# Kernel tuning notes

Measured on AMD Instinct MI355X. Metric: run time of the kernel, lower is better.

## Reference

```python
import jax, jax.numpy as jnp
import numpy as np

# irreps: 128x0e + 64x1o + 32x2e -> blocks of (mul, 2l+1)
MULS_LS = ((128, 0), (64, 1), (32, 2))
NODE_DIM = 128
NUM_IRREPS = 224  # 128+64+32
EQUI_DIM = 480    # 128*1 + 64*3 + 32*5
CONCAT = NODE_DIM + NUM_IRREPS  # 352
EPS = 1e-5
N = 100000


def _blocks(x):
    """Split flat equivariant feature [N, 480] into per-degree blocks [N, mul, 2l+1]."""
    outs, off = [], 0
    for mul, l in MULS_LS:
        d = 2 * l + 1
        outs.append(x[:, off:off + mul * d].reshape(x.shape[0], mul, d))
        off += mul * d
    return outs


def setup_inputs() -> dict:
    key = jax.random.key(0)
    k1, k2, k3, k4 = jax.random.split(key, 4)
    s = 1.0 / np.sqrt(CONCAT)
    return {
        "node_scalar": jax.random.normal(k1, (N, NODE_DIM), jnp.float32),
        "node_equi": jax.random.normal(k2, (N, EQUI_DIM), jnp.float32),
        "ln_w": jnp.ones((NODE_DIM,), jnp.float32),
        "ln_b": jnp.zeros((NODE_DIM,), jnp.float32),
        "W1": jax.random.normal(k3, (CONCAT, CONCAT), jnp.float32) * s,
        "b1": jnp.zeros((CONCAT,), jnp.float32),
        "W2": jax.random.normal(k4, (CONCAT, CONCAT), jnp.float32) * s,
        "b2": jnp.zeros((CONCAT,), jnp.float32),
    }


def reference(node_scalar, node_equi, ln_w, ln_b, W1, b1, W2, b2):
    # ---- scalar LayerNorm ----
    mu = node_scalar.mean(-1, keepdims=True)
    var = node_scalar.var(-1, keepdims=True)
    ns = (node_scalar - mu) * jax.lax.rsqrt(var + EPS) * ln_w + ln_b

    # ---- equivariant LayerNorm: per-degree, mean-centering for l=0, RMS of
    # per-channel norms over the multiplicity axis ----
    eb = []
    for (mul, l), blk in zip(MULS_LS, _blocks(node_equi)):
        if l == 0:
            blk = blk - blk.mean(axis=1, keepdims=True)
        norm2 = (blk * blk).sum(-1, keepdims=True).mean(axis=1, keepdims=True)
        eb.append(blk * jax.lax.rsqrt(norm2 + EPS))

    # ---- EquivariantDot(x, x): per-irrep self dot, component-normalized ----
    inv = jnp.concatenate(
        [(blk * blk).sum(-1) / np.sqrt(2 * l + 1) for (mul, l), blk in zip(MULS_LS, eb)],
        axis=-1)  # [N, 224]

    # ---- concat -> 2-layer gated MLP ----
    cat = jnp.concatenate([ns, inv], axis=-1)  # [N, 352]
    h = jax.nn.silu(cat @ W1 + b1) @ W2 + b2
    d_scalar, gate = h[:, :NODE_DIM], h[:, NODE_DIM:]

    # ---- ElementwiseTensorProduct(equi, gate 0e): per-irrep scalar gating ----
    gparts = jnp.split(gate, [128, 192], axis=-1)  # muls 128, 64, 32
    n = node_scalar.shape[0]
    d_equi = jnp.concatenate(
        [(blk * g[:, :, None]).reshape(n, -1) for blk, g in zip(eb, gparts)],
        axis=-1)  # [N, 480]

    # ---- residual update; concat outputs into one array [N, 608] ----
    return jnp.concatenate([node_scalar + d_scalar, node_equi + d_equi], axis=-1)
```

## Files before the change

### kernel.cpp

```cpp
#include <hip/hip_runtime.h>

#define NODE 128
#define EQUI 480
#define CATD 352
#define OUTD 608
#define RPB  32
#define SA   360
#define NTILES 22
#define KSTEPS 11
#define EPSF 1e-5f

typedef __bf16 bfv8 __attribute__((ext_vector_type(8)));
typedef float  f32x4 __attribute__((ext_vector_type(4)));

__device__ __forceinline__ unsigned short f2bf(float f) {
  unsigned int u = __builtin_bit_cast(unsigned int, f);
  u += 0x7FFFu + ((u >> 16) & 1u);
  return (unsigned short)(u >> 16);
}

__global__ void prep_kernel(const float* __restrict__ W1, const float* __restrict__ W2,
                            unsigned short* __restrict__ WT) {
  int idx = blockIdx.x * 256 + threadIdx.x;
  if (idx >= 2 * CATD * CATD) return;
  int which = (idx >= CATD * CATD);
  int rr = which ? idx - CATD * CATD : idx;
  int j = rr / CATD, k = rr - j * CATD;
  const float* W = which ? W2 : W1;
  WT[idx] = f2bf(W[k * CATD + j]);
}

__global__ __launch_bounds__(256, 2) void fused_kernel(
    const float* __restrict__ node_scalar, const float* __restrict__ node_equi,
    const float* __restrict__ ln_w, const float* __restrict__ ln_b,
    const unsigned short* __restrict__ W1T, const unsigned short* __restrict__ W2T,
    const float* __restrict__ b1, const float* __restrict__ b2,
    float* __restrict__ out, int N) {

  __shared__ __attribute__((aligned(16))) unsigned short sA[RPB * SA];
  __shared__ __attribute__((aligned(16))) unsigned short sH[RPB * SA];
  __shared__ float sMean0[RPB], sS0[RPB], sS1[RPB], sS2[RPB];

  const int tid  = threadIdx.x;
  const long row0 = (long)blockIdx.x * RPB;

  {
    const int r = tid >> 3, g = tid & 7;
    const long row_g = row0 + r;
    if (row_g < N) {
      float lv[16];
      float s = 0.f, q = 0.f;
      const float* xs = node_scalar + row_g * NODE;
      #pragma unroll
      for (int i = 0; i < 4; i++) {
        float4 t = *(const float4*)(xs + g * 16 + i * 4);
        lv[i*4+0] = t.x; lv[i*4+1] = t.y; lv[i*4+2] = t.z; lv[i*4+3] = t.w;
        s += t.x + t.y + t.z + t.w;
        q += t.x*t.x + t.y*t.y + t.z*t.z + t.w*t.w;
      }
      #pragma unroll
      for (int m = 1; m < 8; m <<= 1) { s += __shfl_xor(s, m, 64); q += __shfl_xor(q, m, 64); }
      float mean = s * (1.f / NODE);
      float rstd = rsqrtf(q * (1.f / NODE) - mean * mean + EPSF);
      #pragma unroll
      for (int i = 0; i < 16; i++) {
        int c = g * 16 + i;
        sA[r * SA + c] = f2bf((lv[i] - mean) * rstd * ln_w[c] + ln_b[c]);
      }
      const float* xe = node_equi + row_g * EQUI;
      s = 0.f; q = 0.f;
      #pragma unroll
      for (int i = 0; i < 4; i++) {
        float4 t = *(const float4*)(xe + g * 16 + i * 4);
        lv[i*4+0] = t.x; lv[i*4+1] = t.y; lv[i*4+2] = t.z; lv[i*4+3] = t.w;
        s += t.x + t.y + t.z + t.w;
        q += t.x*t.x + t.y*t.y + t.z*t.z + t.w*t.w;
      }
      #pragma unroll
      for (int m = 1; m < 8; m <<= 1) { s += __shfl_xor(s, m, 64); q += __shfl_xor(q, m, 64); }
      float mean0 = s * (1.f / 128.f);
      float s0 = rsqrtf(q * (1.f / 128.f) - mean0 * mean0 + EPSF);
      #pragma unroll
      for (int i = 0; i < 16; i++) {
        float e = (lv[i] - mean0) * s0;
        sA[r * SA + NODE + g * 16 + i] = f2bf(e * e);
      }
      if (g == 0) { sMean0[r] = mean0; sS0[r] = s0; }
      float a1[24]; q = 0.f;
      #pragma unroll
      for (int i = 0; i < 6; i++) {
        float4 t = *(const float4*)(xe + 128 + g * 24 + i * 4);
        a1[i*4+0] = t.x; a1[i*4+1] = t.y; a1[i*4+2] = t.z; a1[i*4+3] = t.w;
        q += t.x*t.x + t.y*t.y + t.z*t.z + t.w*t.w;
      }
      #pragma unroll
      for (int m = 1; m < 8; m <<= 1) q += __shfl_xor(q, m, 64);
      float s1 = rsqrtf(q * (1.f / 64.f) + EPSF);
      float s1q = s1 * s1 * 0.57735026919f;
      #pragma unroll
      for (int mi = 0; mi < 8; mi++) {
        float ss = a1[mi*3]*a1[mi*3] + a1[mi*3+1]*a1[mi*3+1] + a1[mi*3+2]*a1[mi*3+2];
        sA[r * SA + 256 + g * 8 + mi] = f2bf(ss * s1q);
      }
      if (g == 0) sS1[r] = s1;
      float a2[20]; q = 0.f;
      #pragma unroll
      for (int i = 0; i < 5; i++) {
        float4 t = *(const float4*)(xe + 320 + g * 20 + i * 4);
        a2[i*4+0] = t.x; a2[i*4+1] = t.y; a2[i*4+2] = t.z; a2[i*4+3] = t.w;
        q += t.x*t.x + t.y*t.y + t.z*t.z + t.w*t.w;
      }
      #pragma unroll
      for (int m = 1; m < 8; m <<= 1) q += __shfl_xor(q, m, 64);
      float s2 = rsqrtf(q * (1.f / 32.f) + EPSF);
      float s2q = s2 * s2 * 0.44721359549f;
      #pragma unroll
      for (int mi = 0; mi < 4; mi++) {
        float ss = a2[mi*5]*a2[mi*5] + a2[mi*5+1]*a2[mi*5+1] + a2[mi*5+2]*a2[mi*5+2]
                 + a2[mi*5+3]*a2[mi*5+3] + a2[mi*5+4]*a2[mi*5+4];
        sA[r * SA + 320 + g * 4 + mi] = f2bf(ss * s2q);
      }
      if (g == 0) sS2[r] = s2;
    }
  }
  __syncthreads();

  const int lane = tid & 63, wv = tid >> 6;
  const int ml = lane & 15, quad = lane >> 4;
  const int koff = quad * 8;

  for (int nt = wv; nt < NTILES; nt += 4) {
    f32x4 acc0  = {0.f, 0.f, 0.f, 0.f};
    f32x4 acc1  = {0.f, 0.f, 0.f, 0.f};
    f32x4 acc0b = {0.f, 0.f, 0.f, 0.f};
    f32x4 acc1b = {0.f, 0.f, 0.f, 0.f};
    const unsigned short* Bp = W1T + (nt * 16 + ml) * CATD + koff;
    const unsigned short* A0 = &sA[ml * SA + koff];
    const unsigned short* A1 = &sA[(ml + 16) * SA + koff];
    #pragma unroll
    for (int ks = 0; ks < KSTEPS; ks++) {
      bfv8 b  = *(const bfv8*)(Bp + ks * 32);
      bfv8 a0 = *(const bfv8*)(A0 + ks * 32);
      bfv8 a1 = *(const bfv8*)(A1 + ks * 32);
      if (ks & 1) {
        acc0b = __builtin_amdgcn_mfma_f32_16x16x32_bf16(a0, b, acc0b, 0, 0, 0);
        acc1b = __builtin_amdgcn_mfma_f32_16x16x32_bf16(a1, b, acc1b, 0, 0, 0);
      } else {
        acc0 = __builtin_amdgcn_mfma_f32_16x16x32_bf16(a0, b, acc0, 0, 0, 0);
        acc1 = __builtin_amdgcn_mfma_f32_16x16x32_bf16(a1, b, acc1, 0, 0, 0);
      }
    }
    acc0 += acc0b;
    acc1 += acc1b;
    const int col = nt * 16 + ml;
    const float bb = b1[col];
    #pragma unroll
    for (int reg = 0; reg < 4; reg++) {
      int rr = quad * 4 + reg;
      float v0 = acc0[reg] + bb; v0 = v0 / (1.f + __expf(-v0));
      sH[rr * SA + col] = f2bf(v0);
      float v1 = acc1[reg] + bb; v1 = v1 / (1.f + __expf(-v1));
      sH[(rr + 16) * SA + col] = f2bf(v1);
    }
  }
  __syncthreads();

  for (int nt = wv; nt < NTILES; nt += 4) {
    f32x4 acc0  = {0.f, 0.f, 0.f, 0.f};
    f32x4 acc1  = {0.f, 0.f, 0.f, 0.f};
    f32x4 acc0b = {0.f, 0.f, 0.f, 0.f};
    f32x4 acc1b = {0.f, 0.f, 0.f, 0.f};
    const unsigned short* Bp = W2T + (nt * 16 + ml) * CATD + koff;
    const unsigned short* A0 = &sH[ml * SA + koff];
    const unsigned short* A1 = &sH[(ml + 16) * SA + koff];
    #pragma unroll
    for (int ks = 0; ks < KSTEPS; ks++) {
      bfv8 b  = *(const bfv8*)(Bp + ks * 32);
      bfv8 a0 = *(const bfv8*)(A0 + ks * 32);
      bfv8 a1 = *(const bfv8*)(A1 + ks * 32);
      if (ks & 1) {
        acc0b = __builtin_amdgcn_mfma_f32_16x16x32_bf16(a0, b, acc0b, 0, 0, 0);
        acc1b = __builtin_amdgcn_mfma_f32_16x16x32_bf16(a1, b, acc1b, 0, 0, 0);
      } else {
        acc0 = __builtin_amdgcn_mfma_f32_16x16x32_bf16(a0, b, acc0, 0, 0, 0);
        acc1 = __builtin_amdgcn_mfma_f32_16x16x32_bf16(a1, b, acc1, 0, 0, 0);
      }
    }
    acc0 += acc0b;
    acc1 += acc1b;
    const int col = nt * 16 + ml;
    const float bb = b2[col];
    #pragma unroll
    for (int half = 0; half < 2; half++) {
      #pragma unroll
      for (int reg = 0; reg < 4; reg++) {
        const int r = half * 16 + quad * 4 + reg;
        const long row_g = row0 + r;
        if (row_g >= N) continue;
        float val = (half ? acc1[reg] : acc0[reg]) + bb;
        float* orow = out + row_g * OUTD;
        if (col < 128) {
          orow[col] = node_scalar[row_g * NODE + col] + val;
        } else if (col < 256) {
          const int c = col - 128;
          float x = node_equi[row_g * EQUI + c];
          orow[NODE + c] = x + (x - sMean0[r]) * sS0[r] * val;
        } else if (col < 320) {
          const int i3 = col - 256; const int c0 = 128 + i3 * 3;
          const float f = 1.f + sS1[r] * val;
          #pragma unroll
          for (int d = 0; d < 3; d++) {
            float x = node_equi[row_g * EQUI + c0 + d];
            orow[NODE + c0 + d] = x * f;
          }
        } else {
          const int i5 = col - 320; const int c0 = 320 + i5 * 5;
          const float f = 1.f + sS2[r] * val;
          #pragma unroll
          for (int d = 0; d < 5; d++) {
            float x = node_equi[row_g * EQUI + c0 + d];
            orow[NODE + c0 + d] = x * f;
          }
        }
      }
    }
  }
}

extern "C" void kernel_launch(void* const* d_in, const int* in_sizes, int n_in,
                              void* d_out, int out_size, void* d_ws, size_t ws_size,
                              hipStream_t stream) {
  const float* node_scalar = (const float*)d_in[0];
  const float* node_equi   = (const float*)d_in[1];
  const float* ln_w = (const float*)d_in[2];
  const float* ln_b = (const float*)d_in[3];
  const float* W1   = (const float*)d_in[4];
  const float* b1   = (const float*)d_in[5];
  const float* W2   = (const float*)d_in[6];
  const float* b2   = (const float*)d_in[7];
  float* out = (float*)d_out;
  const int N = in_sizes[0] / NODE;

  unsigned short* WT = (unsigned short*)d_ws;
  const int prep_elems = 2 * CATD * CATD;
  prep_kernel<<<(prep_elems + 255) / 256, 256, 0, stream>>>(W1, W2, WT);

  const int nblk = (N + RPB - 1) / RPB;
  fused_kernel<<<nblk, 256, 0, stream>>>(node_scalar, node_equi, ln_w, ln_b,
                                         WT, WT + CATD * CATD, b1, b2, out, N);
}
```

Baseline: 565.1 us.

## Stage GEMM2 output in LDS and write residual epilogue with coalesced float4 rows

Instead of each MFMA lane scattering its output values to global memory with strided, uncoalesced accesses (especially the 3- and 5-wide equivariant blocks), GEMM2 results plus bias are stored as bf16 into the shared sA buffer. After a barrier, 8 threads per row read node_scalar/node_equi and write the 608-wide output row using contiguous float4 accesses. This targets the memory-bound epilogue at the cost of an extra barrier and bf16 rounding of the second-layer output before the residual add.

```diff
diff --git a/kernel.cpp b/kernel.cpp
--- a/kernel.cpp
+++ b/kernel.cpp
@@ -18,6 +18,12 @@
   u += 0x7FFFu + ((u >> 16) & 1u);
   return (unsigned short)(u >> 16);
 }
+
+__device__ __forceinline__ float bf2f(unsigned short u) {
+  return __builtin_bit_cast(float, (unsigned int)u << 16);
+}
+
+__device__ __forceinline__ float silu_f(float v) { return v / (1.f + __expf(-v)); }
 
 __global__ void prep_kernel(const float* __restrict__ W1, const float* __restrict__ W2,
                             unsigned short* __restrict__ WT) {
@@ -157,9 +163,9 @@
     #pragma unroll
     for (int reg = 0; reg < 4; reg++) {
       int rr = quad * 4 + reg;
-      float v0 = acc0[reg] + bb; v0 = v0 / (1.f + __expf(-v0));
+      float v0 = acc0[reg] + bb; v0 = silu_f(v0);
       sH[rr * SA + col] = f2bf(v0);
-      float v1 = acc1[reg] + bb; v1 = v1 / (1.f + __expf(-v1));
+      float v1 = acc1[reg] + bb; v1 = silu_f(v1);
       sH[(rr + 16) * SA + col] = f2bf(v1);
     }
   }
@@ -191,37 +197,73 @@
     const int col = nt * 16 + ml;
     const float bb = b2[col];
     #pragma unroll
-    for (int half = 0; half < 2; half++) {
-      #pragma unroll
-      for (int reg = 0; reg < 4; reg++) {
-        const int r = half * 16 + quad * 4 + reg;
-        const long row_g = row0 + r;
-        if (row_g >= N) continue;
-        float val = (half ? acc1[reg] : acc0[reg]) + bb;
-        float* orow = out + row_g * OUTD;
-        if (col < 128) {
-          orow[col] = node_scalar[row_g * NODE + col] + val;
-        } else if (col < 256) {
-          const int c = col - 128;
-          float x = node_equi[row_g * EQUI + c];
-          orow[NODE + c] = x + (x - sMean0[r]) * sS0[r] * val;
-        } else if (col < 320) {
-          const int i3 = col - 256; const int c0 = 128 + i3 * 3;
-          const float f = 1.f + sS1[r] * val;
-          #pragma unroll
-          for (int d = 0; d < 3; d++) {
-            float x = node_equi[row_g * EQUI + c0 + d];
-            orow[NODE + c0 + d] = x * f;
-          }
-        } else {
-          const int i5 = col - 320; const int c0 = 320 + i5 * 5;
-          const float f = 1.f + sS2[r] * val;
-          #pragma unroll
-          for (int d = 0; d < 5; d++) {
-            float x = node_equi[row_g * EQUI + c0 + d];
-            orow[NODE + c0 + d] = x * f;
-          }
-        }
+    for (int reg = 0; reg < 4; reg++) {
+      int rr = quad * 4 + reg;
+      sA[rr * SA + col]        = f2bf(acc0[reg] + bb);
+      sA[(rr + 16) * SA + col] = f2bf(acc1[reg] + bb);
+    }
+  }
+  __syncthreads();
+
+  {
+    const int r = tid >> 3, g = tid & 7;
+    const long row_g = row0 + r;
+    if (row_g < N) {
+      const float mean0 = sMean0[r], s0 = sS0[r], s1 = sS1[r], s2 = sS2[r];
+      const float* xs = node_scalar + row_g * NODE;
+      const float* xe = node_equi + row_g * EQUI;
+      float* orow = out + row_g * OUTD;
+      const unsigned short* h2 = &sA[r * SA];
+
+      #pragma unroll
+      for (int i = 0; i < 4; i++) {
+        const int c = g * 16 + i * 4;
+        float4 t = *(const float4*)(xs + c);
+        float4 o;
+        o.x = t.x + bf2f(h2[c + 0]);
+        o.y = t.y + bf2f(h2[c + 1]);
+        o.z = t.z + bf2f(h2[c + 2]);
+        o.w = t.w + bf2f(h2[c + 3]);
+        *(float4*)(orow + c) = o;
+      }
+      #pragma unroll
+      for (int i = 0; i < 4; i++) {
+        const int c = g * 16 + i * 4;
+        float4 t = *(const float4*)(xe + c);
+        float4 o;
+        o.x = t.x + (t.x - mean0) * s0 * bf2f(h2[128 + c + 0]);
+        o.y = t.y + (t.y - mean0) * s0 * bf2f(h2[128 + c + 1]);
+        o.z = t.z + (t.z - mean0) * s0 * bf2f(h2[128 + c + 2]);
+        o.w = t.w + (t.w - mean0) * s0 * bf2f(h2[128 + c + 3]);
+        *(float4*)(orow + 128 + c) = o;
+      }
+      float gv[8];
+      #pragma unroll
+      for (int i = 0; i < 8; i++) gv[i] = 1.f + s1 * bf2f(h2[256 + g * 8 + i]);
+      #pragma unroll
+      for (int i = 0; i < 6; i++) {
+        const int j = g * 24 + i * 4;
+        float4 t = *(const float4*)(xe + 128 + j);
+        float4 o;
+        o.x = t.x * gv[(i * 4 + 0) / 3];
+        o.y = t.y * gv[(i * 4 + 1) / 3];
+        o.z = t.z * gv[(i * 4 + 2) / 3];
+        o.w = t.w * gv[(i * 4 + 3) / 3];
+        *(float4*)(orow + 256 + j) = o;
+      }
+      float hv[4];
+      #pragma unroll
+      for (int i = 0; i < 4; i++) hv[i] = 1.f + s2 * bf2f(h2[320 + g * 4 + i]);
+      #pragma unroll
+      for (int i = 0; i < 5; i++) {
+        const int j = g * 20 + i * 4;
+        float4 t = *(const float4*)(xe + 320 + j);
+        float4 o;
+        o.x = t.x * hv[(i * 4 + 0) / 5];
+        o.y = t.y * hv[(i * 4 + 1) / 5];
+        o.z = t.z * hv[(i * 4 + 2) / 5];
+        o.w = t.w * hv[(i * 4 + 3) / 5];
+        *(float4*)(orow + 448 + j) = o;
       }
     }
   }
```

Measured after the change: 548.2 us. 1.03x faster.
